# Optimization experiments

Hardware: AMD Instinct MI355X
Metric: run time of the kernel (lower is better)

Reference implementation:

```python
import jax, jax.numpy as jnp
import numpy as np

N = 8192        # agents (single node type VEHICLE)
K = 15          # max_Nnode - 1 neighbors per node
E = N * K       # edges
FT = 12         # prediction horizon steps
SD = 4          # state dim (x, y, vx, vy)
ID = 2          # input dim (ax, ay)
ZD = 8          # latent z dim
HE = 256        # history_enc_dim
EE = 128        # edge_enc_dim
OH = 256        # obs_lstm_hidden_dim
GH = 256        # guide_RNN_hidden_dim
FH = 256        # FC_hidden_dim
AD = 16         # att_internal_dim
DT = 0.25
SCALE = 1.0     # input_scale


def setup_inputs() -> dict:
    ks = jax.random.split(jax.random.key(0), 40)
    f = lambda i, s: jax.random.normal(ks[i], s, jnp.float32)
    w = lambda i, s: 0.05 * jax.random.normal(ks[i], s, jnp.float32)
    inp = dict(
        x_last=f(0, (N, SD)), x_st_last=f(1, (N, SD)), hist_enc=f(2, (N, HE)),
        z=f(3, (N, ZD)),
        node_size=jax.random.uniform(ks[4], (N, 2), jnp.float32, 1.0, 3.0),
        W_h0=w(5, (SD, OH)), b_h0=w(6, (OH,)), W_c0=w(7, (SD, OH)), b_c0=w(8, (OH,)),
        W_gh=w(9, (HE + ZD, GH)), b_gh=w(10, (GH,)),
        W_gru_ih=w(11, (HE + ZD, 3 * GH)), W_gru_hh=w(12, (GH, 3 * GH)),
        b_gru_ih=w(13, (3 * GH,)), b_gru_hh=w(14, (3 * GH,)),
        W_proj=w(15, (GH, 2)), b_proj=w(16, (2,)),
        W_att1=w(17, (EE, AD)), W_att2=w(18, (SD, AD)), v_att=w(19, (AD,)),
        W_lstm_ih=w(20, (EE, 4 * OH)), W_lstm_hh=w(21, (OH, 4 * OH)),
        b_lstm_ih=w(22, (4 * OH,)), b_lstm_hh=w(23, (4 * OH,)),
        W_e1=w(24, (SD + 4, FH)), b_e1=w(25, (FH,)), W_e2=w(26, (FH, EE)), b_e2=w(27, (EE,)),
        W_a1=w(28, (OH + ZD + SD + 4, FH)), b_a1=w(29, (FH,)),
        W_a2=w(30, (FH, ID)), b_a2=w(31, (ID,)),
    )
    # edge k is the j-th neighbor of node k // K; index 0 in the enc table is the pad row
    inp["edge_idx1"] = jnp.repeat(jnp.arange(N), K)
    inp["edge_idx2"] = jax.random.randint(ks[32], (E,), 0, N)
    inp["node_obs_idx"] = (jnp.arange(E) + 1).reshape(N, K)
    inp["ft"] = FT
    return inp


def _dyn(s, u):
    # double-integrator: s = [x, y, vx, vy], u = [ax, ay]
    pos = s[:, :2] + s[:, 2:4] * DT + 0.5 * u * DT * DT
    vel = s[:, 2:4] + u * DT
    return jnp.concatenate([pos, vel], -1)


def _forward(x_last, x_st_last, hist_enc, z, node_size,
             W_h0, b_h0, W_c0, b_c0, W_gh, b_gh, W_gru_ih, W_gru_hh, b_gru_ih, b_gru_hh,
             W_proj, b_proj, W_att1, W_att2, v_att, W_lstm_ih, W_lstm_hh, b_lstm_ih, b_lstm_hh,
             W_e1, b_e1, W_e2, b_e2, W_a1, b_a1, W_a2, b_a2,
             edge_idx1, edge_idx2, node_obs_idx, ft):
    n = x_last.shape[0]
    ee = W_e2.shape[1]
    # ---- guide GRU: desired trajectory [ft, N, 2] ----
    xz = jnp.concatenate([hist_enc, z], -1)
    h0g = xz @ W_gh + b_gh
    gi = xz @ W_gru_ih + b_gru_ih  # input is constant over time (xz repeated)
    ir, iz, inn = jnp.split(gi, 3, -1)

    def gru_step(h, _):
        hr, hz, hn = jnp.split(h @ W_gru_hh + b_gru_hh, 3, -1)
        r = jax.nn.sigmoid(ir + hr)
        u = jax.nn.sigmoid(iz + hz)
        nh = (1.0 - u) * jnp.tanh(inn + r * hn) + u * h
        return nh, nh

    _, hs = jax.lax.scan(gru_step, h0g, None, length=ft)
    des = hs @ W_proj + b_proj                       # [ft, N, 2]
    des_next = jnp.concatenate([des[1:], des[-1:]], 0)
    des_prev = jnp.concatenate([jnp.zeros_like(des[:1]), des[:-1]], 0)
    first = jnp.zeros((ft,), jnp.float32).at[0].set(1.0)

    # ---- obs LSTM initial state ----
    h0 = x_st_last @ W_h0 + b_h0
    c0 = x_st_last @ W_c0 + b_c0

    size1 = node_size[edge_idx1]
    size2 = node_size[edge_idx2]
    rad = 0.5 * (jnp.linalg.norm(size1, axis=-1) + jnp.linalg.norm(size2, axis=-1))

    def step(carry, xs):
        prev, prev_st, h, c, terr, ccost = carry
        des_t, des_n, des_p, fst = xs
        # edge gather + collision cost + edge encoding
        s1 = prev[edge_idx1]
        s2 = prev[edge_idx2]
        dist = jnp.linalg.norm(s1[:, :2] - s2[:, :2], axis=-1)
        ccost = ccost + jnp.sum(jax.nn.relu(rad - dist))
        feat = jnp.concatenate([s2 - s1, size1, size2], -1)          # [E, SD+4]
        enc = jax.nn.relu(feat @ W_e1 + b_e1) @ W_e2 + b_e2          # [E, EE]
        enc_all = jnp.concatenate([jnp.zeros((1, ee), enc.dtype), enc], 0)
        obs = enc_all[node_obs_idx]                                   # [N, K, EE]
        # relative state (t==0 uses standardized history directly)
        m = 1.0 - fst
        rel = prev_st - m * x_st_last
        rel = jnp.concatenate([rel[:, :2] - m * des_p, rel[:, 2:]], -1)
        terr = terr + jnp.linalg.norm(rel[:, :2]) / n
        next_wp = des_t - prev_st[:, :2]
        next_wp2 = des_n - prev_st[:, :2]
        # additive attention over neighbors
        scores = jnp.tanh(obs @ W_att1 + (rel @ W_att2)[:, None, :]) @ v_att   # [N, K]
        att = jax.nn.softmax(scores, axis=-1)
        ctx = jnp.einsum('nk,nkd->nd', att, obs)
        # LSTM cell (torch gate order i, f, g, o)
        gates = ctx @ W_lstm_ih + b_lstm_ih + h @ W_lstm_hh + b_lstm_hh
        g_i, g_f, g_g, g_o = jnp.split(gates, 4, -1)
        c = jax.nn.sigmoid(g_f) * c + jax.nn.sigmoid(g_i) * jnp.tanh(g_g)
        h = jax.nn.sigmoid(g_o) * jnp.tanh(c)
        # action net + dynamics rollout
        a_in = jnp.concatenate([h, z, rel, next_wp, next_wp2], -1)   # [N, OH+ZD+SD+4]
        u = SCALE * jnp.tanh(jax.nn.relu(a_in @ W_a1 + b_a1) @ W_a2 + b_a2)
        nxt = _dyn(prev, u)
        nxt_st = _dyn(prev_st, u)
        return (nxt, nxt_st, h, c, terr, ccost), (nxt, u)

    zero = jnp.zeros((), jnp.float32)
    init = (x_last, x_st_last, h0, c0, zero, zero)
    (_, _, _, _, terr, ccost), (state_pred, input_pred) = jax.lax.scan(
        step, init, (des, des_next, des_prev, first))
    return state_pred, input_pred, terr, ccost


def reference(x_last, x_st_last, hist_enc, z, node_size,
              W_h0, b_h0, W_c0, b_c0, W_gh, b_gh, W_gru_ih, W_gru_hh, b_gru_ih, b_gru_hh,
              W_proj, b_proj, W_att1, W_att2, v_att, W_lstm_ih, W_lstm_hh, b_lstm_ih, b_lstm_hh,
              W_e1, b_e1, W_e2, b_e2, W_a1, b_a1, W_a2, b_a2,
              edge_idx1, edge_idx2, node_obs_idx, ft):
    return _forward(x_last, x_st_last, hist_enc, z, node_size,
                    W_h0, b_h0, W_c0, b_c0, W_gh, b_gh, W_gru_ih, W_gru_hh, b_gru_ih, b_gru_hh,
                    W_proj, b_proj, W_att1, W_att2, v_att, W_lstm_ih, W_lstm_hh, b_lstm_ih, b_lstm_hh,
                    W_e1, b_e1, W_e2, b_e2, W_a1, b_a1, W_a2, b_a2,
                    edge_idx1, edge_idx2, node_obs_idx, ft)
```

## Files before the change

kernel.cpp:

```cpp
#include <hip/hip_runtime.h>

#define DEVI __device__ __forceinline__

constexpr int N_  = 8192;
constexpr int K_  = 15;
constexpr int E_  = N_ * K_;
constexpr int FTS = 12;
constexpr float DT_ = 0.25f;

typedef __attribute__((ext_vector_type(8))) short short8x;
typedef __attribute__((ext_vector_type(4))) float float4x;

union U8 { unsigned int u[4]; short8x v; };

DEVI float sigf(float x) { return 1.0f / (1.0f + __expf(-x)); }
DEVI float tanhf_fast(float x) { float e = __expf(2.f * x); return 1.f - 2.f / (e + 1.f); }
DEVI unsigned int f2u(float x) { union { float f; unsigned int u; } c; c.f = x; return c.u; }
DEVI float u2f(unsigned int x) { union { unsigned int u; float f; } c; c.u = x; return c.f; }

DEVI void split8(const float* __restrict__ s, short8x& hi8, short8x& lo8) {
  U8 ph, pl;
#pragma unroll
  for (int p = 0; p < 4; p++) {
    float a0 = s[2*p], a1 = s[2*p+1];
    unsigned int u0 = f2u(a0), u1 = f2u(a1);
    unsigned int h0 = u0 & 0xFFFF0000u, h1 = u1 & 0xFFFF0000u;
    ph.u[p] = (u0 >> 16) | h1;
    float l0 = a0 - u2f(h0), l1 = a1 - u2f(h1);
    pl.u[p] = (f2u(l0) >> 16) | (f2u(l1) & 0xFFFF0000u);
  }
  hi8 = ph.v; lo8 = pl.v;
}

__global__ void k_zero(float* ss) {
  ss[blockIdx.x * 256 + threadIdx.x] = 0.f;
}

__global__ __launch_bounds__(256) void k_edge_static(
    const int* __restrict__ e1, const int* __restrict__ e2,
    const float* __restrict__ nsize, float* __restrict__ rad, float* __restrict__ szf)
{
  int e = blockIdx.x * 256 + threadIdx.x;
  if (e >= E_) return;
  int i1 = e1[e], i2 = e2[e];
  float s1x = nsize[i1*2+0], s1y = nsize[i1*2+1];
  float s2x = nsize[i2*2+0], s2y = nsize[i2*2+1];
  rad[e] = 0.5f * (sqrtf(s1x*s1x + s1y*s1y) + sqrtf(s2x*s2x + s2y*s2y));
  *(float4*)&szf[e*4] = make_float4(s1x, s1y, s2x, s2y);
}

__global__ __launch_bounds__(256) void k_prep_hi(
    const float* __restrict__ W, unsigned short* __restrict__ out)
{
  int t = blockIdx.x * 256 + threadIdx.x;
  int fid = t >> 6, L = t & 63;
  int ks = fid >> 3, nt = fid & 7;
  int k0 = ks * 32 + (L >> 4) * 8;
  int n  = nt * 16 + (L & 15);
  unsigned int hi[4];
#pragma unroll
  for (int p = 0; p < 4; p++) {
    float w0 = W[(size_t)(k0 + 2*p) * 128 + n];
    float w1 = W[(size_t)(k0 + 2*p + 1) * 128 + n];
    hi[p] = (f2u(w0) >> 16) | (f2u(w1) & 0xFFFF0000u);
  }
  *(uint4*)(out + (size_t)fid * 512 + (size_t)L * 8) = make_uint4(hi[0], hi[1], hi[2], hi[3]);
}

__global__ __launch_bounds__(256) void k_prep1(
    const float* __restrict__ WA, const float* __restrict__ WB,
    int mode, int split, int wA, int wB, int Ktot, int NT, int nfrag,
    unsigned short* __restrict__ out)
{
  int t = blockIdx.x * 256 + threadIdx.x;
  int fid = t >> 6, L = t & 63;
  if (fid >= nfrag) return;
  int ks = fid / NT, nt = fid % NT;
  int k0 = ks * 32 + (L >> 4) * 8;
  int n  = nt * 16 + (L & 15);
  unsigned int hi[4];
#pragma unroll
  for (int p = 0; p < 4; p++) {
    float w0 = 0.f, w1 = 0.f;
    int ka = k0 + 2*p, kb = ka + 1;
    if (mode == 0) {
      if (ka < Ktot) w0 = (ka < split) ? WA[(size_t)ka*wA + n] : WB[(size_t)(ka-split)*wB + n];
      if (kb < Ktot) w1 = (kb < split) ? WA[(size_t)kb*wA + n] : WB[(size_t)(kb-split)*wB + n];
    } else {
      if (ka < Ktot) w0 = (n < split) ? WA[(size_t)ka*wA + n] : WB[(size_t)ka*wB + (n-split)];
      if (kb < Ktot) w1 = (n < split) ? WA[(size_t)kb*wA + n] : WB[(size_t)kb*wB + (n-split)];
    }
    hi[p] = (f2u(w0) >> 16) | (f2u(w1) & 0xFFFF0000u);
  }
  *(uint4*)(out + (size_t)fid * 512 + (size_t)L * 8) = make_uint4(hi[0], hi[1], hi[2], hi[3]);
}

__global__ __launch_bounds__(256) void k_xz_mfma(
    const float* __restrict__ hist, const float* __restrict__ z,
    const unsigned short* __restrict__ wB,
    const float* __restrict__ b_gh, const float* __restrict__ b_gih,
    float* __restrict__ gh0, unsigned int* __restrict__ gi_ru,
    float* __restrict__ gi_n)
{
  __shared__ __align__(16) float Abuf[2][64][36];
  const int tid = threadIdx.x;
  const int w = tid >> 6, lane = tid & 63;
  const int m = lane & 15, q = lane >> 4;
  const int n0 = blockIdx.x * 64;
  const int r_ = tid >> 2, c_ = (tid & 3) * 8;
  float4x acc[16];
#pragma unroll
  for (int tl = 0; tl < 16; tl++) acc[tl] = (float4x){0.f,0.f,0.f,0.f};

  auto LD = [&](int ks, float4& v0, float4& v1) {
    int kk = ks*32 + c_;
    int n = n0 + r_;
    if (kk < 256) {
      v0 = *(const float4*)&hist[(size_t)n*256 + kk];
      v1 = *(const float4*)&hist[(size_t)n*256 + kk + 4];
    } else if (kk == 256) {
      v0 = *(const float4*)&z[n*8];
      v1 = *(const float4*)&z[n*8 + 4];
    } else {
      v0 = make_float4(0,0,0,0); v1 = v0;
    }
  };
  {
    float4 v0, v1; LD(0, v0, v1);
    *(float4*)&Abuf[0][r_][c_]     = v0;
    *(float4*)&Abuf[0][r_][c_ + 4] = v1;
  }
  __syncthreads();
  for (int ks = 0; ks < 9; ks++) {
    float4 v0, v1;
    if (ks < 8) LD(ks + 1, v0, v1);
    short8x aHi, aLo;
    split8(&Abuf[ks & 1][w*16 + m][q*8], aHi, aLo);
#pragma unroll
    for (int tl = 0; tl < 16; tl++) {
      int nt = blockIdx.y*16 + tl;
      size_t off = (size_t)(ks*64 + nt) * 512 + (size_t)lane*8;
      short8x bh = *(const short8x*)(wB + off);
      acc[tl] = __builtin_amdgcn_mfma_f32_16x16x32_bf16(aLo, bh, acc[tl], 0, 0, 0);
      acc[tl] = __builtin_amdgcn_mfma_f32_16x16x32_bf16(aHi, bh, acc[tl], 0, 0, 0);
    }
    if (ks < 8) {
      *(float4*)&Abuf[(ks+1) & 1][r_][c_]     = v0;
      *(float4*)&Abuf[(ks+1) & 1][r_][c_ + 4] = v1;
      __syncthreads();
    }
  }
#pragma unroll
  for (int tl = 0; tl < 16; tl++) {
    int col = (blockIdx.y*16 + tl)*16 + m;
    float bias = (col < 256) ? b_gh[col] : b_gih[col - 256];
#pragma unroll
    for (int i = 0; i < 4; i++) {
      int n = n0 + w*16 + q*4 + i;
      float v = acc[tl][i] + bias;
      if (col < 256) {
        gh0[(size_t)n*256 + col] = v;
      } else {
        int cj = col - 256;
        int gate = cj >> 8, j = cj & 255;
        if (gate == 2) gi_n[(size_t)n*256 + j] = v;
        else ((unsigned short*)gi_ru)[((size_t)n*256 + j)*2 + gate] =
               (unsigned short)(f2u(v) >> 16);
      }
    }
  }
}

__global__ __launch_bounds__(1024) void k_gru_all(
    const float* __restrict__ gh0, const unsigned short* __restrict__ wB,
    const float* __restrict__ b_ghh,
    const unsigned int* __restrict__ gi_ru, const float* __restrict__ gi_n,
    const float* __restrict__ W_proj, const float* __restrict__ b_proj,
    float* __restrict__ des)
{
  __shared__ __align__(16) float h_lds[32][260];
  __shared__ float sm_des[8][32][2];
  const int tid = threadIdx.x;
  const int w = tid >> 6, lane = tid & 63;
  const int m = lane & 15, q = lane >> 4;
  const int rh = w & 1, jh = w >> 1;
  const int n0 = blockIdx.x * 32;

  {
    int r = tid >> 5, c = (tid & 31) * 8;
    const float4* src = (const float4*)&gh0[(size_t)(n0 + r)*256 + c];
    float4 v0 = src[0], v1 = src[1];
    *(float4*)&h_lds[r][c]     = v0;
    *(float4*)&h_lds[r][c + 4] = v1;
  }
  float br_[2], bz_[2], bn_[2], wp0_[2], wp1_[2];
#pragma unroll
  for (int jt = 0; jt < 2; jt++) {
    int j = jh*32 + jt*16 + m;
    br_[jt] = b_ghh[j];
    bz_[jt] = b_ghh[256 + j];
    bn_[jt] = b_ghh[512 + j];
    wp0_[jt] = W_proj[j*2];
    wp1_[jt] = W_proj[j*2 + 1];
  }
  const float bp0 = b_proj[0], bp1 = b_proj[1];
  float ir_[2][4], iz_[2][4], inn_[2][4];
#pragma unroll
  for (int jt = 0; jt < 2; jt++) {
    int j = jh*32 + jt*16 + m;
#pragma unroll
    for (int i = 0; i < 4; i++) {
      int rl = rh*16 + q*4 + i;
      unsigned int ru = gi_ru[(size_t)(n0 + rl)*256 + j];
      ir_[jt][i]  = u2f(ru << 16);
      iz_[jt][i]  = u2f(ru & 0xFFFF0000u);
      inn_[jt][i] = gi_n[(size_t)(n0 + rl)*256 + j];
    }
  }
  const unsigned short* __restrict__ wLane = wB + (size_t)lane * 8;
  __syncthreads();

#pragma unroll 1
  for (int t = 0; t < FTS; t++) {
    float4x acc[6];
#pragma unroll
    for (int tl = 0; tl < 6; tl++) acc[tl] = (float4x){0.f,0.f,0.f,0.f};

#pragma unroll 2
    for (int ks = 0; ks < 8; ks++) {
      float a8[8];
      {
        const float* hp = &h_lds[rh*16 + m][ks*32 + q*8];
        float4 v0 = *(const float4*)hp;
        float4 v1 = *(const float4*)(hp + 4);
        a8[0]=v0.x; a8[1]=v0.y; a8[2]=v0.z; a8[3]=v0.w;
        a8[4]=v1.x; a8[5]=v1.y; a8[6]=v1.z; a8[7]=v1.w;
      }
      short8x aHi, aLo;
      split8(a8, aHi, aLo);
#pragma unroll
      for (int tl = 0; tl < 6; tl++) {
        int g = tl >> 1, jt = tl & 1;
        int nt = g*16 + jh*2 + jt;
        short8x bh = *(const short8x*)(wLane + (size_t)(ks*48 + nt) * 512);
        acc[tl] = __builtin_amdgcn_mfma_f32_16x16x32_bf16(aLo, bh, acc[tl], 0, 0, 0);
        acc[tl] = __builtin_amdgcn_mfma_f32_16x16x32_bf16(aHi, bh, acc[tl], 0, 0, 0);
      }
    }
    __syncthreads();
    float pd0[4] = {0,0,0,0}, pd1[4] = {0,0,0,0};
#pragma unroll
    for (int jt = 0; jt < 2; jt++) {
      int j = jh*32 + jt*16 + m;
#pragma unroll
      for (int i = 0; i < 4; i++) {
        int rl = rh*16 + q*4 + i;
        float hold = h_lds[rl][j];
        float r = sigf(ir_[jt][i] + acc[0*2 + jt][i] + br_[jt]);
        float u = sigf(iz_[jt][i] + acc[1*2 + jt][i] + bz_[jt]);
        float nh = (1.f - u) * tanhf_fast(inn_[jt][i] + r * (acc[2*2 + jt][i] + bn_[jt])) + u * hold;
        h_lds[rl][j] = nh;
        pd0[i] += nh * wp0_[jt];
        pd1[i] += nh * wp1_[jt];
      }
    }
#pragma unroll
    for (int off = 1; off < 16; off <<= 1) {
#pragma unroll
      for (int i = 0; i < 4; i++) {
        pd0[i] += __shfl_xor(pd0[i], off);
        pd1[i] += __shfl_xor(pd1[i], off);
      }
    }
    if (m == 0) {
#pragma unroll
      for (int i = 0; i < 4; i++) {
        sm_des[jh][rh*16 + q*4 + i][0] = pd0[i];
        sm_des[jh][rh*16 + q*4 + i][1] = pd1[i];
      }
    }
    __syncthreads();
    if (tid < 64) {
      int r = tid >> 1, c = tid & 1;
      float s = 0.f;
#pragma unroll
      for (int k8 = 0; k8 < 8; k8++) s += sm_des[k8][r][c];
      des[((size_t)t * N_ + n0 + r) * 2 + c] = s + (c ? bp1 : bp0);
    }
  }
}

__global__ __launch_bounds__(256) void k_lstm_mfma(
    const float* __restrict__ ctxg, const float* __restrict__ h_in,
    const unsigned short* __restrict__ wB,
    const float* __restrict__ b_ih, const float* __restrict__ b_hh,
    float* __restrict__ c_st, float* __restrict__ h_out)
{
  __shared__ __align__(16) float Abuf[2][64][36];
  const int tid = threadIdx.x;
  const int w = tid >> 6, lane = tid & 63;
  const int m = lane & 15, q = lane >> 4;
  const int n0 = blockIdx.x * 64;
  const int j0 = blockIdx.y * 32;
  const int r_ = tid >> 2, c_ = (tid & 3) * 8;
  float4x acc[8];
#pragma unroll
  for (int tl = 0; tl < 8; tl++) acc[tl] = (float4x){0.f,0.f,0.f,0.f};

  auto LD = [&](int ks, float4& v0, float4& v1) {
    int kk = ks*32 + c_;
    int n = n0 + r_;
    if (kk < 128) {
      v0 = *(const float4*)&ctxg[(size_t)n*128 + kk];
      v1 = *(const float4*)&ctxg[(size_t)n*128 + kk + 4];
    } else {
      v0 = *(const float4*)&h_in[(size_t)n*256 + kk - 128];
      v1 = *(const float4*)&h_in[(size_t)n*256 + kk - 124];
    }
  };
  {
    float4 v0, v1; LD(0, v0, v1);
    *(float4*)&Abuf[0][r_][c_]     = v0;
    *(float4*)&Abuf[0][r_][c_ + 4] = v1;
  }
  __syncthreads();
  for (int ks = 0; ks < 12; ks++) {
    float4 v0, v1;
    if (ks < 11) LD(ks + 1, v0, v1);
    short8x aHi, aLo;
    split8(&Abuf[ks & 1][w*16 + m][q*8], aHi, aLo);
#pragma unroll
    for (int tl = 0; tl < 8; tl++) {
      int g = tl >> 1, jt = tl & 1;
      int nt = g*16 + (j0 >> 4) + jt;
      size_t off = (size_t)(ks*64 + nt) * 512 + (size_t)lane*8;
      short8x bh = *(const short8x*)(wB + off);
      acc[tl] = __builtin_amdgcn_mfma_f32_16x16x32_bf16(aLo, bh, acc[tl], 0, 0, 0);
      acc[tl] = __builtin_amdgcn_mfma_f32_16x16x32_bf16(aHi, bh, acc[tl], 0, 0, 0);
    }
    if (ks < 11) {
      *(float4*)&Abuf[(ks+1) & 1][r_][c_]     = v0;
      *(float4*)&Abuf[(ks+1) & 1][r_][c_ + 4] = v1;
      __syncthreads();
    }
  }
#pragma unroll
  for (int jt = 0; jt < 2; jt++) {
    int j = j0 + jt*16 + m;
    float bi = b_ih[j]       + b_hh[j];
    float bf = b_ih[256 + j] + b_hh[256 + j];
    float bg = b_ih[512 + j] + b_hh[512 + j];
    float bo = b_ih[768 + j] + b_hh[768 + j];
#pragma unroll
    for (int i = 0; i < 4; i++) {
      int n = n0 + w*16 + q*4 + i;
      float g_i = sigf(acc[0*2 + jt][i] + bi);
      float g_f = sigf(acc[1*2 + jt][i] + bf);
      float g_g = tanhf_fast(acc[2*2 + jt][i] + bg);
      float g_o = sigf(acc[3*2 + jt][i] + bo);
      float cv = g_f * c_st[(size_t)n*256 + j] + g_i * g_g;
      c_st[(size_t)n*256 + j] = cv;
      h_out[(size_t)n*256 + j] = g_o * tanhf_fast(cv);
    }
  }
}

__global__ __launch_bounds__(256) void k_action_mfma(
    const float* __restrict__ h, const float* __restrict__ z,
    const float* __restrict__ rel, const float* __restrict__ nwp, const float* __restrict__ nwp2,
    const unsigned short* __restrict__ wB, const float* __restrict__ b_a1,
    const float* __restrict__ W_a2, const float* __restrict__ b_a2,
    float* __restrict__ prev, float* __restrict__ prev_st,
    float* __restrict__ outS, float* __restrict__ outU)
{
  __shared__ __align__(16) float Abuf[2][32][36];
  __shared__ float sm_p[2][16][2];
  const int tid = threadIdx.x;
  const int w = tid >> 6, lane = tid & 63;
  const int m = lane & 15, q = lane >> 4;
  const int ng = w >> 1, hh = w & 1;
  const int n0 = blockIdx.x * 32;
  const int r_ = tid >> 3, c_ = (tid & 7) * 4;
  float4x acc[8];
#pragma unroll
  for (int j = 0; j < 8; j++) acc[j] = (float4x){0.f,0.f,0.f,0.f};

  auto LD = [&](int ks) -> float4 {
    int kk = ks*32 + c_;
    int n = n0 + r_;
    float4 v;
    if (kk < 256)       v = *(const float4*)&h[(size_t)n*256 + kk];
    else if (kk == 256) v = *(const float4*)&z[n*8];
    else if (kk == 260) v = *(const float4*)&z[n*8 + 4];
    else if (kk == 264) v = *(const float4*)&rel[n*4];
    else if (kk == 268) {
      float2 w1 = *(const float2*)&nwp[n*2];
      float2 w2 = *(const float2*)&nwp2[n*2];
      v = make_float4(w1.x, w1.y, w2.x, w2.y);
    } else v = make_float4(0,0,0,0);
    return v;
  };
  {
    float4 v = LD(0);
    *(float4*)&Abuf[0][r_][c_] = v;
  }
  __syncthreads();
  for (int ks = 0; ks < 9; ks++) {
    float4 v;
    if (ks < 8) v = LD(ks + 1);
    short8x aHi, aLo;
    split8(&Abuf[ks & 1][ng*16 + m][q*8], aHi, aLo);
#pragma unroll
    for (int j = 0; j < 8; j++) {
      int tl = hh*8 + j;
      size_t off = (size_t)(ks*16 + tl) * 512 + (size_t)lane*8;
      short8x bh = *(const short8x*)(wB + off);
      acc[j] = __builtin_amdgcn_mfma_f32_16x16x32_bf16(aLo, bh, acc[j], 0, 0, 0);
      acc[j] = __builtin_amdgcn_mfma_f32_16x16x32_bf16(aHi, bh, acc[j], 0, 0, 0);
    }
    if (ks < 8) {
      *(float4*)&Abuf[(ks+1) & 1][r_][c_] = v;
      __syncthreads();
    }
  }
  float p0[4] = {0,0,0,0}, p1[4] = {0,0,0,0};
#pragma unroll
  for (int j = 0; j < 8; j++) {
    int col = (hh*8 + j)*16 + m;
    float ba = b_a1[col];
    float2 w2 = *(const float2*)&W_a2[col*2];
#pragma unroll
    for (int i = 0; i < 4; i++) {
      float hv = fmaxf(acc[j][i] + ba, 0.f);
      p0[i] += hv * w2.x;
      p1[i] += hv * w2.y;
    }
  }
#pragma unroll
  for (int off = 1; off < 16; off <<= 1) {
#pragma unroll
    for (int i = 0; i < 4; i++) {
      p0[i] += __shfl_xor(p0[i], off);
      p1[i] += __shfl_xor(p1[i], off);
    }
  }
  if (hh == 1 && m == 0) {
#pragma unroll
    for (int i = 0; i < 4; i++) {
      sm_p[ng][q*4 + i][0] = p0[i];
      sm_p[ng][q*4 + i][1] = p1[i];
    }
  }
  __syncthreads();
  if (hh == 0 && m == 0) {
    float ba0 = b_a2[0], ba1 = b_a2[1];
    const float hd = 0.5f * DT_ * DT_;
#pragma unroll
    for (int i = 0; i < 4; i++) {
      int n = n0 + ng*16 + q*4 + i;
      float ux = tanhf_fast(p0[i] + sm_p[ng][q*4 + i][0] + ba0);
      float uy = tanhf_fast(p1[i] + sm_p[ng][q*4 + i][1] + ba1);
      float4 pv = *(const float4*)&prev[n*4];
      float4 ps = *(const float4*)&prev_st[n*4];
      float4 npv, nps;
      npv.x = pv.x + pv.z*DT_ + ux*hd;
      npv.y = pv.y + pv.w*DT_ + uy*hd;
      npv.z = pv.z + ux*DT_;
      npv.w = pv.w + uy*DT_;
      nps.x = ps.x + ps.z*DT_ + ux*hd;
      nps.y = ps.y + ps.w*DT_ + uy*hd;
      nps.z = ps.z + ux*DT_;
      nps.w = ps.w + uy*DT_;
      *(float4*)&prev[n*4] = npv;
      *(float4*)&prev_st[n*4] = nps;
      *(float4*)&outS[(size_t)n*4] = npv;
      outU[n*2]     = ux;
      outU[n*2 + 1] = uy;
    }
  }
}

__global__ __launch_bounds__(256) void k_init_hc(
    const float* __restrict__ x_last, const float* __restrict__ x_st_last,
    const float* __restrict__ W_h0, const float* __restrict__ b_h0,
    const float* __restrict__ W_c0, const float* __restrict__ b_c0,
    float* __restrict__ h, float* __restrict__ c,
    float* __restrict__ prev, float* __restrict__ prev_st)
{
  const int n = blockIdx.x;
  const int j = threadIdx.x;
  float x0 = x_st_last[n*4], x1 = x_st_last[n*4+1], x2 = x_st_last[n*4+2], x3 = x_st_last[n*4+3];
  h[(size_t)n*256 + j] = b_h0[j] + x0*W_h0[j] + x1*W_h0[256+j] + x2*W_h0[512+j] + x3*W_h0[768+j];
  c[(size_t)n*256 + j] = b_c0[j] + x0*W_c0[j] + x1*W_c0[256+j] + x2*W_c0[512+j] + x3*W_c0[768+j];
  if (j < 4) prev[n*4 + j] = x_last[n*4 + j];
  else if (j < 8) prev_st[n*4 + (j-4)] = x_st_last[n*4 + (j-4)];
}

__global__ __launch_bounds__(256, 4) void k_edge(
    const float* __restrict__ prev, const float* __restrict__ prev_st,
    const float* __restrict__ x_st_last,
    const float* __restrict__ szf, const float* __restrict__ rad,
    const int* __restrict__ nobs, const int* __restrict__ e1, const int* __restrict__ e2,
    const float* __restrict__ W_e1, const float* __restrict__ b_e1,
    const unsigned short* __restrict__ wsB, const float* __restrict__ b_e2,
    const unsigned short* __restrict__ wattA, const float* __restrict__ W_att2,
    const float* __restrict__ v_att,
    const float* __restrict__ des_p, const float* __restrict__ des_t,
    const float* __restrict__ des_n,
    float* __restrict__ relg, float* __restrict__ nwp, float* __restrict__ nwp2,
    float* __restrict__ ctx, float* __restrict__ ss_t, float* __restrict__ cc)
{
  __shared__ __align__(16) float smem[4776];
  const int tid = threadIdx.x;
  const int eb = blockIdx.x;

  float* sm_stage = smem;
  float* sm_feats = smem + 4096;
  float* sm_flags = smem + 4608;
  float* sm_relv  = smem + 4672;
  float* sm_watt2 = smem + 4688;
  float* sm_vatt  = smem + 4752;
  float* sm_red   = smem + 4768;

  const int n0  = eb * 4;
  const int slot = (eb & 15) << 4;
  const int lane = tid & 63;
  const int g    = tid >> 6;
  const int q = lane >> 4, m = lane & 15;

  if (tid >= 176 && tid < 192) sm_vatt[tid - 176] = v_att[tid - 176];
  if (tid >= 192) sm_watt2[tid - 192] = W_att2[tid - 192];

  if (tid < 64) {
    float v = 0.f;
    if (tid < 60) {
      int gg = tid / 15, k = tid % 15;
      int idx = nobs[(n0 + gg) * 15 + k];
      float f[8] = {0,0,0,0,0,0,0,0};
      float fl = 0.f;
      if (idx > 0) {
        int e = idx - 1;
        int i1 = e1[e], i2 = e2[e];
#pragma unroll
        for (int d = 0; d < 4; d++) f[d] = prev[i2*4 + d] - prev[i1*4 + d];
        float4 sz = *(const float4*)&szf[(size_t)e*4];
        f[4] = sz.x; f[5] = sz.y; f[6] = sz.z; f[7] = sz.w;
        fl = 1.f;
        float dist = sqrtf(f[0]*f[0] + f[1]*f[1]);
        v = fmaxf(rad[e] - dist, 0.f);
      }
#pragma unroll
      for (int d = 0; d < 8; d++) sm_feats[(gg*16 + k)*8 + d] = f[d];
      sm_flags[gg*16 + k] = fl;
    } else {
      int gg = tid - 60;
#pragma unroll
      for (int d = 0; d < 8; d++) sm_feats[(gg*16 + 15)*8 + d] = 0.f;
      sm_flags[gg*16 + 15] = 0.f;
    }
#pragma unroll
    for (int off = 32; off; off >>= 1) v += __shfl_down(v, off);
    if (tid == 0) atomicAdd(cc + slot, v);
  } else if (tid < 68) {
    int gg = tid - 64;
    int n = n0 + gg;
    float4 ps = *(const float4*)&prev_st[n*4];
    float r0, r1, r2, r3;
    if (des_p) {
      float4 xs = *(const float4*)&x_st_last[n*4];
      r0 = ps.x - xs.x - des_p[n*2];
      r1 = ps.y - xs.y - des_p[n*2 + 1];
      r2 = ps.z - xs.z;
      r3 = ps.w - xs.w;
    } else { r0 = ps.x; r1 = ps.y; r2 = ps.z; r3 = ps.w; }
    sm_relv[gg*4+0] = r0; sm_relv[gg*4+1] = r1; sm_relv[gg*4+2] = r2; sm_relv[gg*4+3] = r3;
    *(float4*)&relg[n*4] = make_float4(r0, r1, r2, r3);
    nwp[n*2]      = des_t[n*2]     - ps.x;
    nwp[n*2 + 1]  = des_t[n*2 + 1] - ps.y;
    nwp2[n*2]     = des_n[n*2]     - ps.x;
    nwp2[n*2 + 1] = des_n[n*2 + 1] - ps.y;
    sm_red[gg] = r0*r0 + r1*r1;
  }
  {
    const uint4* src = (const uint4*)wsB;
    uint4* dst = (uint4*)sm_stage;
    dst[tid]       = src[tid];
    dst[tid + 256] = src[tid + 256];
  }
  __syncthreads();
  if (tid == 64) atomicAdd(ss_t + slot, sm_red[0] + sm_red[1] + sm_red[2] + sm_red[3]);

  float f[8];
  {
    const float4 fa = *(const float4*)&sm_feats[(g*16 + m)*8];
    const float4 fb = *(const float4*)&sm_feats[(g*16 + m)*8 + 4];
    f[0]=fa.x; f[1]=fa.y; f[2]=fa.z; f[3]=fa.w; f[4]=fb.x; f[5]=fb.y; f[6]=fb.z; f[7]=fb.w;
  }
  float4x encR[8];
#pragma unroll
  for (int nt = 0; nt < 8; nt++) encR[nt] = (float4x){0.f,0.f,0.f,0.f};
  const float4* We14 = (const float4*)W_e1;
  const float4* Be14 = (const float4*)b_e1;

  for (int ks = 0; ks < 8; ks++) {
    uint4 r0, r1;
    if (ks < 7) {
      const uint4* src = (const uint4*)wsB + (ks + 1) * 512;
      r0 = src[tid];
      r1 = src[tid + 256];
    }
    short8x aHi, aLo;
    {
      float h8[8];
      float4 b0 = Be14[8*ks + 2*q];
      float4 b1 = Be14[8*ks + 2*q + 1];
      h8[0]=b0.x; h8[1]=b0.y; h8[2]=b0.z; h8[3]=b0.w; h8[4]=b1.x; h8[5]=b1.y; h8[6]=b1.z; h8[7]=b1.w;
#pragma unroll
      for (int d = 0; d < 8; d++) {
        float4 wa = We14[d*64 + ks*8 + 2*q];
        float4 wb = We14[d*64 + ks*8 + 2*q + 1];
        h8[0] += f[d]*wa.x; h8[1] += f[d]*wa.y; h8[2] += f[d]*wa.z; h8[3] += f[d]*wa.w;
        h8[4] += f[d]*wb.x; h8[5] += f[d]*wb.y; h8[6] += f[d]*wb.z; h8[7] += f[d]*wb.w;
      }
#pragma unroll
      for (int p = 0; p < 8; p++) h8[p] = fmaxf(h8[p], 0.f);
      split8(h8, aHi, aLo);
    }
    const unsigned short* sb = (const unsigned short*)sm_stage + (ks & 1) * 4096;
#pragma unroll
    for (int nt = 0; nt < 8; nt++) {
      short8x bh = *(const short8x*)(sb + nt*512 + lane*8);
      encR[nt] = __builtin_amdgcn_mfma_f32_16x16x32_bf16(aLo, bh, encR[nt], 0, 0, 0);
      encR[nt] = __builtin_amdgcn_mfma_f32_16x16x32_bf16(aHi, bh, encR[nt], 0, 0, 0);
    }
    if (ks < 7) {
      uint4* dst = (uint4*)sm_stage + ((ks + 1) & 1) * 512;
      dst[tid]       = r0;
      dst[tid + 256] = r1;
      __syncthreads();
    }
  }
  float4x fl4 = *(const float4x*)&sm_flags[g*16 + q*4];
#pragma unroll
  for (int nt = 0; nt < 8; nt++) {
    float b2 = b_e2[nt*16 + m];
#pragma unroll
    for (int i = 0; i < 4; i++) encR[nt][i] = (encR[nt][i] + b2) * fl4[i];
  }

  __syncthreads();
  {
  }
  float* tb = sm_stage + g * 576;
  float4x sacc = {0.f, 0.f, 0.f, 0.f};
#pragma unroll
  for (int ksc = 0; ksc < 4; ksc++) {
#pragma unroll
    for (int ntl = 0; ntl < 2; ntl++) {
#pragma unroll
      for (int i = 0; i < 4; i++)
        tb[(q*4 + i)*36 + ntl*16 + m] = encR[2*ksc + ntl][i];
    }
    __builtin_amdgcn_s_waitcnt(0);
    float a8[8];
    {
      const float4* tp = (const float4*)(tb + m*36 + q*8);
      float4 t0 = tp[0], t1 = tp[1];
      a8[0]=t0.x; a8[1]=t0.y; a8[2]=t0.z; a8[3]=t0.w;
      a8[4]=t1.x; a8[5]=t1.y; a8[6]=t1.z; a8[7]=t1.w;
    }
    __builtin_amdgcn_s_waitcnt(0);
    short8x aH, aL;
    split8(a8, aH, aL);
    short8x bh = *(const short8x*)(wattA + ksc*512 + lane*8);
    sacc = __builtin_amdgcn_mfma_f32_16x16x32_bf16(aL, bh, sacc, 0, 0, 0);
    sacc = __builtin_amdgcn_mfma_f32_16x16x32_bf16(aH, bh, sacc, 0, 0, 0);
  }

  float relw;
  {
    float4 rv = *(const float4*)&sm_relv[g*4];
    relw = rv.x * sm_watt2[m] + rv.y * sm_watt2[16 + m]
         + rv.z * sm_watt2[32 + m] + rv.w * sm_watt2[48 + m];
  }
  float vat = sm_vatt[m];
  float val[4];
#pragma unroll
  for (int i = 0; i < 4; i++) val[i] = tanhf_fast(sacc[i] + relw) * vat;
#pragma unroll
  for (int msk = 1; msk < 16; msk <<= 1) {
#pragma unroll
    for (int i = 0; i < 4; i++) val[i] += __shfl_xor(val[i], msk);
  }
  if (q == 3) val[3] = -3.0e38f;
  float mx = fmaxf(fmaxf(val[0], val[1]), fmaxf(val[2], val[3]));
  mx = fmaxf(mx, __shfl_xor(mx, 16));
  mx = fmaxf(mx, __shfl_xor(mx, 32));
  float4x ev;
  float ssum = 0.f;
#pragma unroll
  for (int i = 0; i < 4; i++) { ev[i] = __expf(val[i] - mx); ssum += ev[i]; }
  ssum += __shfl_xor(ssum, 16);
  ssum += __shfl_xor(ssum, 32);
  float inv = 1.f / ssum;
#pragma unroll
  for (int i = 0; i < 4; i++) ev[i] *= inv;

  float cpart[8];
#pragma unroll
  for (int nt = 0; nt < 8; nt++) {
    float cv = ev[0]*encR[nt][0] + ev[1]*encR[nt][1] + ev[2]*encR[nt][2] + ev[3]*encR[nt][3];
    cv += __shfl_xor(cv, 16);
    cv += __shfl_xor(cv, 32);
    cpart[nt] = cv;
  }
  float v0 = (q == 0) ? cpart[0] : (q == 1) ? cpart[2] : (q == 2) ? cpart[4] : cpart[6];
  float v1 = (q == 0) ? cpart[1] : (q == 1) ? cpart[3] : (q == 2) ? cpart[5] : cpart[7];
  size_t cb = (size_t)(n0 + g) * 128 + q*32 + m;
  ctx[cb]      = v0;
  ctx[cb + 16] = v1;
}

__global__ void k_final(const float* __restrict__ ss, float* __restrict__ out) {
  const int lane = threadIdx.x;
  float red[13];
#pragma unroll
  for (int a = 0; a < 13; a++) {
    float v = (lane < 16) ? ss[a*256 + lane*16] : 0.f;
    v += __shfl_xor(v, 1);
    v += __shfl_xor(v, 2);
    v += __shfl_xor(v, 4);
    v += __shfl_xor(v, 8);
    red[a] = v;
  }
  if (lane == 0) {
    float t = 0.f;
    for (int i = 0; i < FTS; i++) t += sqrtf(red[i]);
    out[(size_t)FTS * N_ * 6]     = t / (float)N_;
    out[(size_t)FTS * N_ * 6 + 1] = red[12];
  }
}

extern "C" void kernel_launch(void* const* d_in, const int* in_sizes, int n_in,
                              void* d_out, int out_size, void* d_ws, size_t ws_size,
                              hipStream_t stream) {
  (void)in_sizes; (void)n_in; (void)out_size; (void)ws_size;
  const float* x_last    = (const float*)d_in[0];
  const float* x_st_last = (const float*)d_in[1];
  const float* hist_enc  = (const float*)d_in[2];
  const float* z         = (const float*)d_in[3];
  const float* node_size = (const float*)d_in[4];
  const float* W_h0 = (const float*)d_in[5];
  const float* b_h0 = (const float*)d_in[6];
  const float* W_c0 = (const float*)d_in[7];
  const float* b_c0 = (const float*)d_in[8];
  const float* W_gh = (const float*)d_in[9];
  const float* b_gh = (const float*)d_in[10];
  const float* W_gih = (const float*)d_in[11];
  const float* W_ghh = (const float*)d_in[12];
  const float* b_gih = (const float*)d_in[13];
  const float* b_ghh = (const float*)d_in[14];
  const float* W_proj = (const float*)d_in[15];
  const float* b_proj = (const float*)d_in[16];
  const float* W_att1 = (const float*)d_in[17];
  const float* W_att2 = (const float*)d_in[18];
  const float* v_att  = (const float*)d_in[19];
  const float* W_lih = (const float*)d_in[20];
  const float* W_lhh = (const float*)d_in[21];
  const float* b_lih = (const float*)d_in[22];
  const float* b_lhh = (const float*)d_in[23];
  const float* W_e1 = (const float*)d_in[24];
  const float* b_e1 = (const float*)d_in[25];
  const float* W_e2 = (const float*)d_in[26];
  const float* b_e2 = (const float*)d_in[27];
  const float* W_a1 = (const float*)d_in[28];
  const float* b_a1 = (const float*)d_in[29];
  const float* W_a2 = (const float*)d_in[30];
  const float* b_a2 = (const float*)d_in[31];
  const int* e1   = (const int*)d_in[32];
  const int* e2   = (const int*)d_in[33];
  const int* nobs = (const int*)d_in[34];
  float* out = (float*)d_out;

  float* wsf     = (float*)d_ws;
  float* prev    = wsf;
  float* prev_st = wsf + 32768;
  float* des     = wsf + 65536;
  float* rad     = wsf + 262160;
  float* szf     = wsf + 385040;
  float* baseA   = wsf + 876560;
  float* gh0           = baseA;
  unsigned int* gi_ru  = (unsigned int*)(baseA + (size_t)2 * N_ * 256);
  float* gi_n          = baseA + (size_t)3 * N_ * 256;
  float* hA   = baseA;
  float* hB   = baseA + (size_t)N_ * 256;
  float* cbuf = baseA + (size_t)2 * N_ * 256;
  float* ctx  = baseA + (size_t)3 * N_ * 256;
  float* rel  = baseA + (size_t)4 * N_ * 256;
  float* nwp  = rel + (size_t)N_ * 4;
  float* nwp2 = nwp + (size_t)N_ * 2;
  unsigned short* wsBe = (unsigned short*)(wsf + 11362320);
  unsigned short* wsBg = (unsigned short*)(wsf + 11427856);
  unsigned short* wsBl = (unsigned short*)(wsf + 11624464);
  unsigned short* wsBx = (unsigned short*)(wsf + 12017680);
  unsigned short* wsBa = (unsigned short*)(wsf + 12312592);
  unsigned short* wattA = (unsigned short*)(wsf + 12386320);
  float* ssx = wsf + 12388368;

  k_zero<<<13, 256, 0, stream>>>(ssx);
  k_edge_static<<<(E_ + 255) / 256, 256, 0, stream>>>(e1, e2, node_size, rad, szf);

  k_prep_hi<<<16, 256, 0, stream>>>(W_e2, wsBe);
  k_prep1<<<96,  256, 0, stream>>>(W_ghh, W_ghh, 0, 256, 768,  768,  256, 48, 384, wsBg);
  k_prep1<<<192, 256, 0, stream>>>(W_lih, W_lhh, 0, 128, 1024, 1024, 384, 64, 768, wsBl);
  k_prep1<<<144, 256, 0, stream>>>(W_gh,  W_gih, 1, 256, 256,  768,  264, 64, 576, wsBx);
  k_prep1<<<36,  256, 0, stream>>>(W_a1,  W_a1,  0, 272, 256,  256,  272, 16, 144, wsBa);
  k_prep1<<<1,   256, 0, stream>>>(W_att1, W_att1, 0, 128, 16, 16, 128, 1, 4, wattA);

  k_xz_mfma<<<dim3(128, 4), 256, 0, stream>>>(hist_enc, z, wsBx, b_gh, b_gih,
                                              gh0, gi_ru, gi_n);
  k_gru_all<<<256, 1024, 0, stream>>>(gh0, wsBg, b_ghh, gi_ru, gi_n,
                                      W_proj, b_proj, des);

  k_init_hc<<<N_, 256, 0, stream>>>(x_last, x_st_last, W_h0, b_h0, W_c0, b_c0,
                                    hA, cbuf, prev, prev_st);
  float* hcur = hA;
  float* hnxt = hB;
  for (int t = 0; t < FTS; t++) {
    const float* des_t = des + (size_t)t * N_ * 2;
    const float* des_n = des + (size_t)((t + 1 < FTS) ? t + 1 : FTS - 1) * N_ * 2;
    const float* des_p = (t > 0) ? des + (size_t)(t - 1) * N_ * 2 : nullptr;
    k_edge<<<2048, 256, 0, stream>>>(prev, prev_st, x_st_last, szf, rad,
                                     nobs, e1, e2, W_e1, b_e1, wsBe, b_e2,
                                     wattA, W_att2, v_att,
                                     des_p, des_t, des_n,
                                     rel, nwp, nwp2, ctx,
                                     ssx + (size_t)t * 256, ssx + 12 * 256);
    k_lstm_mfma<<<dim3(128, 8), 256, 0, stream>>>(ctx, hcur, wsBl, b_lih, b_lhh,
                                                  cbuf, hnxt);
    k_action_mfma<<<256, 256, 0, stream>>>(hnxt, z, rel, nwp, nwp2,
                                           wsBa, b_a1, W_a2, b_a2,
                                           prev, prev_st,
                                           out + (size_t)t * N_ * 4,
                                           out + (size_t)FTS * N_ * 4 + (size_t)t * N_ * 2);
    float* tmp = hcur; hcur = hnxt; hnxt = tmp;
  }
  k_final<<<1, 64, 0, stream>>>(ssx, out);
}
```

Baseline: 1.405 ms.

## Store GRU hidden state pre-split as bf16 hi/lo and drop LDS staging in LSTM/edge kernels

The GRU kernel now keeps its hidden state in shared memory as separate bf16 high and low halves, so the split into hi/lo operands is done once per update instead of on every MFMA operand load. The LSTM kernel loads A operands straight from global memory into registers instead of double-buffering them through shared memory with barriers. The edge-encoder kernel reads weight fragments directly from global memory per lane rather than staging them cooperatively in LDS. These changes remove syncthreads and LDS traffic, but rely on cache hits for repeated global loads and slightly change how the old hidden value is rebuilt in the GRU.

```diff
diff --git a/kernel.cpp b/kernel.cpp
--- a/kernel.cpp
+++ b/kernel.cpp
@@ -178,7 +178,8 @@
     const float* __restrict__ W_proj, const float* __restrict__ b_proj,
     float* __restrict__ des)
 {
-  __shared__ __align__(16) float h_lds[32][260];
+  __shared__ __align__(16) unsigned short h_hi[32][264];
+  __shared__ __align__(16) unsigned short h_lo[32][264];
   __shared__ float sm_des[8][32][2];
   const int tid = threadIdx.x;
   const int w = tid >> 6, lane = tid & 63;
@@ -188,10 +189,15 @@
 
   {
     int r = tid >> 5, c = (tid & 31) * 8;
+    float a8[8];
     const float4* src = (const float4*)&gh0[(size_t)(n0 + r)*256 + c];
     float4 v0 = src[0], v1 = src[1];
-    *(float4*)&h_lds[r][c]     = v0;
-    *(float4*)&h_lds[r][c + 4] = v1;
+    a8[0]=v0.x; a8[1]=v0.y; a8[2]=v0.z; a8[3]=v0.w;
+    a8[4]=v1.x; a8[5]=v1.y; a8[6]=v1.z; a8[7]=v1.w;
+    short8x hi8, lo8;
+    split8(a8, hi8, lo8);
+    *(short8x*)&h_hi[r][c] = hi8;
+    *(short8x*)&h_lo[r][c] = lo8;
   }
   float br_[2], bz_[2], bn_[2], wp0_[2], wp1_[2];
 #pragma unroll
@@ -228,16 +234,8 @@
 
 #pragma unroll 2
     for (int ks = 0; ks < 8; ks++) {
-      float a8[8];
-      {
-        const float* hp = &h_lds[rh*16 + m][ks*32 + q*8];
-        float4 v0 = *(const float4*)hp;
-        float4 v1 = *(const float4*)(hp + 4);
-        a8[0]=v0.x; a8[1]=v0.y; a8[2]=v0.z; a8[3]=v0.w;
-        a8[4]=v1.x; a8[5]=v1.y; a8[6]=v1.z; a8[7]=v1.w;
-      }
-      short8x aHi, aLo;
-      split8(a8, aHi, aLo);
+      short8x aHi = *(const short8x*)&h_hi[rh*16 + m][ks*32 + q*8];
+      short8x aLo = *(const short8x*)&h_lo[rh*16 + m][ks*32 + q*8];
 #pragma unroll
       for (int tl = 0; tl < 6; tl++) {
         int g = tl >> 1, jt = tl & 1;
@@ -255,11 +253,16 @@
 #pragma unroll
       for (int i = 0; i < 4; i++) {
         int rl = rh*16 + q*4 + i;
-        float hold = h_lds[rl][j];
+        float hold = u2f(((unsigned int)h_hi[rl][j]) << 16)
+                   + u2f(((unsigned int)h_lo[rl][j]) << 16);
         float r = sigf(ir_[jt][i] + acc[0*2 + jt][i] + br_[jt]);
         float u = sigf(iz_[jt][i] + acc[1*2 + jt][i] + bz_[jt]);
         float nh = (1.f - u) * tanhf_fast(inn_[jt][i] + r * (acc[2*2 + jt][i] + bn_[jt])) + u * hold;
-        h_lds[rl][j] = nh;
+        unsigned int un = f2u(nh);
+        unsigned int uh = un & 0xFFFF0000u;
+        float lo = nh - u2f(uh);
+        h_hi[rl][j] = (unsigned short)(un >> 16);
+        h_lo[rl][j] = (unsigned short)(f2u(lo) >> 16);
         pd0[i] += nh * wp0_[jt];
         pd1[i] += nh * wp1_[jt];
       }
@@ -296,39 +299,30 @@
     const float* __restrict__ b_ih, const float* __restrict__ b_hh,
     float* __restrict__ c_st, float* __restrict__ h_out)
 {
-  __shared__ __align__(16) float Abuf[2][64][36];
   const int tid = threadIdx.x;
   const int w = tid >> 6, lane = tid & 63;
   const int m = lane & 15, q = lane >> 4;
   const int n0 = blockIdx.x * 64;
   const int j0 = blockIdx.y * 32;
-  const int r_ = tid >> 2, c_ = (tid & 3) * 8;
+  const int row = n0 + w*16 + m;
+  const float* __restrict__ crow = ctxg + (size_t)row*128 + q*8;
+  const float* __restrict__ hrow = h_in + (size_t)row*256 + q*8;
   float4x acc[8];
 #pragma unroll
   for (int tl = 0; tl < 8; tl++) acc[tl] = (float4x){0.f,0.f,0.f,0.f};
 
-  auto LD = [&](int ks, float4& v0, float4& v1) {
-    int kk = ks*32 + c_;
-    int n = n0 + r_;
-    if (kk < 128) {
-      v0 = *(const float4*)&ctxg[(size_t)n*128 + kk];
-      v1 = *(const float4*)&ctxg[(size_t)n*128 + kk + 4];
-    } else {
-      v0 = *(const float4*)&h_in[(size_t)n*256 + kk - 128];
-      v1 = *(const float4*)&h_in[(size_t)n*256 + kk - 124];
-    }
-  };
-  {
-    float4 v0, v1; LD(0, v0, v1);
-    *(float4*)&Abuf[0][r_][c_]     = v0;
-    *(float4*)&Abuf[0][r_][c_ + 4] = v1;
-  }
-  __syncthreads();
+#pragma unroll 2
   for (int ks = 0; ks < 12; ks++) {
-    float4 v0, v1;
-    if (ks < 11) LD(ks + 1, v0, v1);
+    float a8[8];
+    {
+      const float* src = (ks < 4) ? (crow + ks*32) : (hrow + (ks - 4)*32);
+      float4 v0 = *(const float4*)src;
+      float4 v1 = *(const float4*)(src + 4);
+      a8[0]=v0.x; a8[1]=v0.y; a8[2]=v0.z; a8[3]=v0.w;
+      a8[4]=v1.x; a8[5]=v1.y; a8[6]=v1.z; a8[7]=v1.w;
+    }
     short8x aHi, aLo;
-    split8(&Abuf[ks & 1][w*16 + m][q*8], aHi, aLo);
+    split8(a8, aHi, aLo);
 #pragma unroll
     for (int tl = 0; tl < 8; tl++) {
       int g = tl >> 1, jt = tl & 1;
@@ -337,11 +331,6 @@
       short8x bh = *(const short8x*)(wB + off);
       acc[tl] = __builtin_amdgcn_mfma_f32_16x16x32_bf16(aLo, bh, acc[tl], 0, 0, 0);
       acc[tl] = __builtin_amdgcn_mfma_f32_16x16x32_bf16(aHi, bh, acc[tl], 0, 0, 0);
-    }
-    if (ks < 11) {
-      *(float4*)&Abuf[(ks+1) & 1][r_][c_]     = v0;
-      *(float4*)&Abuf[(ks+1) & 1][r_][c_ + 4] = v1;
-      __syncthreads();
     }
   }
 #pragma unroll
@@ -581,12 +570,6 @@
     nwp2[n*2 + 1] = des_n[n*2 + 1] - ps.y;
     sm_red[gg] = r0*r0 + r1*r1;
   }
-  {
-    const uint4* src = (const uint4*)wsB;
-    uint4* dst = (uint4*)sm_stage;
-    dst[tid]       = src[tid];
-    dst[tid + 256] = src[tid + 256];
-  }
   __syncthreads();
   if (tid == 64) atomicAdd(ss_t + slot, sm_red[0] + sm_red[1] + sm_red[2] + sm_red[3]);
 
@@ -601,14 +584,10 @@
   for (int nt = 0; nt < 8; nt++) encR[nt] = (float4x){0.f,0.f,0.f,0.f};
   const float4* We14 = (const float4*)W_e1;
   const float4* Be14 = (const float4*)b_e1;
-
+  const unsigned short* __restrict__ wLane = wsB + (size_t)lane * 8;
+
+#pragma unroll 2
   for (int ks = 0; ks < 8; ks++) {
-    uint4 r0, r1;
-    if (ks < 7) {
-      const uint4* src = (const uint4*)wsB + (ks + 1) * 512;
-      r0 = src[tid];
-      r1 = src[tid + 256];
-    }
     short8x aHi, aLo;
     {
       float h8[8];
@@ -626,19 +605,12 @@
       for (int p = 0; p < 8; p++) h8[p] = fmaxf(h8[p], 0.f);
       split8(h8, aHi, aLo);
     }
-    const unsigned short* sb = (const unsigned short*)sm_stage + (ks & 1) * 4096;
 #pragma unroll
     for (int nt = 0; nt < 8; nt++) {
-      short8x bh = *(const short8x*)(sb + nt*512 + lane*8);
+      short8x bh = *(const short8x*)(wLane + (size_t)(ks*8 + nt) * 512);
       encR[nt] = __builtin_amdgcn_mfma_f32_16x16x32_bf16(aLo, bh, encR[nt], 0, 0, 0);
       encR[nt] = __builtin_amdgcn_mfma_f32_16x16x32_bf16(aHi, bh, encR[nt], 0, 0, 0);
     }
-    if (ks < 7) {
-      uint4* dst = (uint4*)sm_stage + ((ks + 1) & 1) * 512;
-      dst[tid]       = r0;
-      dst[tid + 256] = r1;
-      __syncthreads();
-    }
   }
   float4x fl4 = *(const float4x*)&sm_flags[g*16 + q*4];
 #pragma unroll
@@ -648,9 +620,6 @@
     for (int i = 0; i < 4; i++) encR[nt][i] = (encR[nt][i] + b2) * fl4[i];
   }
 
-  __syncthreads();
-  {
-  }
   float* tb = sm_stage + g * 576;
   float4x sacc = {0.f, 0.f, 0.f, 0.f};
 #pragma unroll
```

New measurement: 1.721 ms. 22.4% more time.
